# Optimization experiments

Measured on AMD Instinct MI355X. Metric: run time of the kernel, lower is better.

The kernel has to match this reference:

```python
import jax, jax.numpy as jnp
import numpy as np

EMBED_DIM = 768
N_HEADS = 12
TIME_RATIO = 0.5
HEAD_DIM = EMBED_DIM // N_HEADS          # 64
T_HEAD = int(HEAD_DIM * TIME_RATIO)      # 32 time dims per head
T_DIM = T_HEAD * N_HEADS                 # 384 time dims overall
EPS = 1e-5


def _ln(v, g, b):
    m = jnp.mean(v, axis=-1, keepdims=True)
    var = jnp.mean((v - m) ** 2, axis=-1, keepdims=True)
    return (v - m) * jax.lax.rsqrt(var + EPS) * g + b


def minkowski_ln(x, g_t, b_t, g_s, b_s):
    # normalize time-like and space-like channel groups separately
    xt, xs = x[..., :T_DIM], x[..., T_DIM:]
    return jnp.concatenate([_ln(xt, g_t, b_t), _ln(xs, g_s, b_s)], axis=-1)


def lorentz_attention(x, Wq, bq, Wk, bk, Wv, bv, Wo, bo):
    B, S, D = x.shape
    def heads(W, b):
        return (x @ W + b).reshape(B, S, N_HEADS, HEAD_DIM).transpose(0, 2, 1, 3)
    q, k, v = heads(Wq, bq), heads(Wk, bk), heads(Wv, bv)
    # Minkowski metric signature (-,...,-,+,...,+) within each head
    eta = jnp.concatenate([-jnp.ones((T_HEAD,), x.dtype), jnp.ones((HEAD_DIM - T_HEAD,), x.dtype)])
    logits = jnp.einsum('bhqd,bhkd->bhqk', q * eta, k) / np.sqrt(HEAD_DIM).astype(np.float32)
    attn = jax.nn.softmax(logits, axis=-1)
    o = jnp.einsum('bhqk,bhkd->bhqd', attn, v)
    o = o.transpose(0, 2, 1, 3).reshape(B, S, D)
    return o @ Wo + bo


def setup_inputs() -> dict:
    key = jax.random.key(0)
    ks = jax.random.split(key, 16)
    D, H4 = EMBED_DIM, EMBED_DIM * 4
    s = 0.02
    inp = {
        'x': jax.random.normal(ks[0], (2, 2048, D), jnp.float32),
        'Wq': jax.random.normal(ks[1], (D, D), jnp.float32) * s, 'bq': jnp.zeros((D,), jnp.float32),
        'Wk': jax.random.normal(ks[2], (D, D), jnp.float32) * s, 'bk': jnp.zeros((D,), jnp.float32),
        'Wv': jax.random.normal(ks[3], (D, D), jnp.float32) * s, 'bv': jnp.zeros((D,), jnp.float32),
        'Wo': jax.random.normal(ks[4], (D, D), jnp.float32) * s, 'bo': jnp.zeros((D,), jnp.float32),
        'g1t': jnp.ones((T_DIM,), jnp.float32), 'b1t': jnp.zeros((T_DIM,), jnp.float32),
        'g1s': jnp.ones((D - T_DIM,), jnp.float32), 'b1s': jnp.zeros((D - T_DIM,), jnp.float32),
        'W1': jax.random.normal(ks[5], (D, H4), jnp.float32) * s, 'bb1': jnp.zeros((H4,), jnp.float32),
        'W2': jax.random.normal(ks[6], (H4, D), jnp.float32) * s, 'bb2': jnp.zeros((D,), jnp.float32),
        'g2t': jnp.ones((T_DIM,), jnp.float32), 'b2t': jnp.zeros((T_DIM,), jnp.float32),
        'g2s': jnp.ones((D - T_DIM,), jnp.float32), 'b2s': jnp.zeros((D - T_DIM,), jnp.float32),
    }
    return inp


def reference(x, Wq, bq, Wk, bk, Wv, bv, Wo, bo,
              g1t, b1t, g1s, b1s, W1, bb1, W2, bb2,
              g2t, b2t, g2s, b2s):
    a = lorentz_attention(x, Wq, bq, Wk, bk, Wv, bv, Wo, bo)
    x = minkowski_ln(x + a, g1t, b1t, g1s, b1s)
    h = jax.nn.gelu(x @ W1 + bb1) @ W2 + bb2
    x = minkowski_ln(x + h, g2t, b2t, g2s, b2s)
    return x
```

## Files before the change

### kernel.cpp

```cpp
#include <hip/hip_runtime.h>
#include <cstddef>
#include <cstdint>

#define D_EMB  768
#define NHEAD  12
#define HDIM   64
#define THEAD  32
#define SEQ    2048
#define BATCH  2
#define NROW   (BATCH*SEQ)
#define HID4   3072

typedef unsigned short u16;
typedef __bf16 bf16x8 __attribute__((ext_vector_type(8)));
typedef float  f32x4  __attribute__((ext_vector_type(4)));
typedef unsigned short u16x8 __attribute__((ext_vector_type(8)));

__device__ __forceinline__ u16 f2bf(float f) {
    unsigned u = __builtin_bit_cast(unsigned, f);
    return (u16)((u + 0x7FFFu + ((u >> 16) & 1u)) >> 16);
}
__device__ __forceinline__ float bf2f(u16 h) {
    return __builtin_bit_cast(float, (unsigned)h << 16);
}

__device__ __forceinline__ void gload_lds16(const void* g, void* l) {
    __builtin_amdgcn_global_load_lds(
        reinterpret_cast<const __attribute__((address_space(1))) void*>(
            reinterpret_cast<uintptr_t>(g)),
        reinterpret_cast<__attribute__((address_space(3))) void*>(
            (uint32_t)reinterpret_cast<uintptr_t>(l)),
        16, 0, 0);
}

__device__ __forceinline__ void tcast(float (*t)[33], const float* __restrict__ W,
                                      u16* __restrict__ WT, int K, int M,
                                      int mt, int kt)
{
    const int m0 = mt * 32, k0 = kt * 32;
    const int tx = threadIdx.x & 31, ty = threadIdx.x >> 5;
#pragma unroll
    for (int i = 0; i < 32; i += 8)
        t[ty + i][tx] = W[(size_t)(k0 + ty + i) * M + m0 + tx];
    __syncthreads();
#pragma unroll
    for (int i = 0; i < 32; i += 8)
        WT[(size_t)(m0 + ty + i) * K + k0 + tx] = f2bf(t[tx][ty + i]);
}

__global__ __launch_bounds__(256)
void prep(const float* __restrict__ Wq, const float* __restrict__ Wk,
          const float* __restrict__ Wv, const float* __restrict__ Wo,
          const float* __restrict__ W1, const float* __restrict__ W2,
          const float* __restrict__ bq, const float* __restrict__ bk,
          const float* __restrict__ bv, const float* __restrict__ x,
          u16* __restrict__ WqkvoT, u16* __restrict__ W1T,
          u16* __restrict__ W2T, u16* __restrict__ xb,
          float* __restrict__ bqkv)
{
    __shared__ float t[32][33];
    const int bid = blockIdx.x;
    if (bid < 2304) {
        const int z = bid / 576, r = bid % 576;
        const float* W = z == 0 ? Wq : z == 1 ? Wk : z == 2 ? Wv : Wo;
        tcast(t, W, WqkvoT + (size_t)z * 768 * 768, 768, 768, r % 24, r / 24);
    } else if (bid < 4608) {
        const int r = bid - 2304;
        tcast(t, W1, W1T, 768, 3072, r % 96, r / 96);
    } else if (bid < 6912) {
        const int r = bid - 4608;
        tcast(t, W2, W2T, 3072, 768, r % 24, r / 24);
    } else if (bid < 8448) {
        const int i = (bid - 6912) * 2048 + threadIdx.x * 8;
        const float4 a = *reinterpret_cast<const float4*>(x + i);
        const float4 b = *reinterpret_cast<const float4*>(x + i + 4);
        u16x8 h;
        h[0] = f2bf(a.x); h[1] = f2bf(a.y); h[2] = f2bf(a.z); h[3] = f2bf(a.w);
        h[4] = f2bf(b.x); h[5] = f2bf(b.y); h[6] = f2bf(b.z); h[7] = f2bf(b.w);
        *reinterpret_cast<u16x8*>(xb + i) = h;
    } else {
        const int i = (bid - 8448) * 256 + threadIdx.x;
        if (i < 2304)
            bqkv[i] = i < 768 ? bq[i] : (i < 1536 ? bk[i - 768] : bv[i - 1536]);
    }
}

template<int EPI>
__global__ __launch_bounds__(256)
void gemm_bf16(const u16* __restrict__ A, const u16* __restrict__ B,
               const float* __restrict__ bias, void* __restrict__ Cp,
               u16* __restrict__ VTp, int K, int N)
{
    __shared__ u16 As[2][128 * 32];
    __shared__ u16 Bs[2][128 * 32];
    const int tid  = threadIdx.x;
    const int lane = tid & 63;
    const int w    = tid >> 6;
    const int m0 = blockIdx.x * 128, n0 = blockIdx.y * 128;
    const int wr = (w >> 1) << 6, wc = (w & 1) << 6;

    const int seg0 = (w << 11) + lane * 16;
    const int row0 = seg0 >> 6, cb0 = (seg0 & 63) >> 1;
    const int seg1 = seg0 + 1024;
    const int row1 = seg1 >> 6, cb1 = (seg1 & 63) >> 1;
    const u16* a0 = A + (size_t)(m0 + row0) * K + cb0;
    const u16* a1 = A + (size_t)(m0 + row1) * K + cb1;
    const u16* b0 = B + (size_t)(n0 + row0) * K + cb0;
    const u16* b1 = B + (size_t)(n0 + row1) * K + cb1;
    const int lo0 = (w * 2 + 0) << 9;
    const int lo1 = (w * 2 + 1) << 9;

    int aIdx[4], bIdx[4];
#pragma unroll
    for (int i = 0; i < 4; ++i) {
        aIdx[i] = (wr + i * 16 + (lane & 15)) * 32 + ((lane >> 4) << 3);
        bIdx[i] = (wc + i * 16 + (lane & 15)) * 32 + ((lane >> 4) << 3);
    }

    f32x4 acc[4][4];
#pragma unroll
    for (int i = 0; i < 4; ++i)
#pragma unroll
        for (int j = 0; j < 4; ++j)
#pragma unroll
            for (int q = 0; q < 4; ++q) acc[i][j][q] = 0.f;

    gload_lds16(a0, &As[0][lo0]);
    gload_lds16(a1, &As[0][lo1]);
    gload_lds16(b0, &Bs[0][lo0]);
    gload_lds16(b1, &Bs[0][lo1]);
    __syncthreads();

    int cur = 0;
    for (int k0 = 0; k0 < K; k0 += 32) {
        if (k0 + 32 < K) {
            gload_lds16(a0 + k0 + 32, &As[cur ^ 1][lo0]);
            gload_lds16(a1 + k0 + 32, &As[cur ^ 1][lo1]);
            gload_lds16(b0 + k0 + 32, &Bs[cur ^ 1][lo0]);
            gload_lds16(b1 + k0 + 32, &Bs[cur ^ 1][lo1]);
        }
        bf16x8 af[4], bv[4];
#pragma unroll
        for (int i = 0; i < 4; ++i)
            af[i] = *reinterpret_cast<const bf16x8*>(&As[cur][aIdx[i]]);
#pragma unroll
        for (int j = 0; j < 4; ++j)
            bv[j] = *reinterpret_cast<const bf16x8*>(&Bs[cur][bIdx[j]]);
#pragma unroll
        for (int i = 0; i < 4; ++i)
#pragma unroll
            for (int j = 0; j < 4; ++j)
                acc[i][j] = __builtin_amdgcn_mfma_f32_16x16x32_bf16(
                    af[i], bv[j], acc[i][j], 0, 0, 0);
        __syncthreads();
        cur ^= 1;
    }

#pragma unroll
    for (int i = 0; i < 4; ++i) {
#pragma unroll
        for (int q = 0; q < 4; ++q) {
            const int row = m0 + wr + i * 16 + ((lane >> 4) << 2) + q;
#pragma unroll
            for (int j = 0; j < 4; ++j) {
                const int col = n0 + wc + j * 16 + (lane & 15);
                float v = acc[i][j][q] + bias[col];
                if (EPI == 2) {
                    const float u3 = v * v * v;
                    v = 0.5f * v * (1.f + tanhf(0.7978845608028654f *
                                                (v + 0.044715f * u3)));
                    ((u16*)Cp)[(size_t)row * N + col] = f2bf(v);
                } else {
                    if (n0 < 1536) {
                        ((u16*)Cp)[(size_t)row * 1536 + col] = f2bf(v);
                    } else {
                        const int c2 = col - 1536;
                        const int hh = c2 >> 6, dd = c2 & 63;
                        const int bb = row >> 11, tok = row & 2047;
                        const int t = tok & 63;
                        const int p = ((t & 15) << 2) | (t >> 4);
                        VTp[((size_t)(bb * NHEAD + hh) * HDIM + dd) * SEQ
                            + (tok & ~63) + p] = f2bf(v);
                    }
                }
            }
        }
    }
}

__global__ __launch_bounds__(256)
void gemm_n64(const u16* __restrict__ A, const u16* __restrict__ B,
              const float* __restrict__ bias, float* __restrict__ C0,
              float* __restrict__ C1, int Khalf, int Ktot, int N)
{
    __shared__ u16 As[2][64 * 32];
    __shared__ u16 Bs[2][128 * 32];
    const int tid  = threadIdx.x;
    const int lane = tid & 63;
    const int w    = tid >> 6;
    const int l15  = lane & 15;
    const int g    = lane >> 4;
    const int m0 = blockIdx.x * 64, n0 = blockIdx.y * 128;
    const int zz = blockIdx.z;
    const int kbase = zz * Khalf;
    float* __restrict__ C = zz ? C1 : C0;

    const int segA = (w << 10) + lane * 16;
    const int rowA = segA >> 6, cbA = (segA & 63) >> 1;
    const u16* aP = A + (size_t)(m0 + rowA) * Ktot + kbase + cbA;
    const int loA = w << 9;
    const int seg0 = (w << 11) + lane * 16;
    const int row0 = seg0 >> 6, cb0 = (seg0 & 63) >> 1;
    const int seg1 = seg0 + 1024;
    const int row1 = seg1 >> 6, cb1 = (seg1 & 63) >> 1;
    const u16* b0 = B + (size_t)(n0 + row0) * Ktot + kbase + cb0;
    const u16* b1 = B + (size_t)(n0 + row1) * Ktot + kbase + cb1;
    const int lo0 = w << 10, lo1 = (w << 10) + 512;

    int aIdx[4], bIdx[2];
#pragma unroll
    for (int i = 0; i < 4; ++i) aIdx[i] = (i * 16 + l15) * 32 + (g << 3);
#pragma unroll
    for (int j = 0; j < 2; ++j) bIdx[j] = ((w << 5) + j * 16 + l15) * 32 + (g << 3);

    f32x4 acc[4][2];
#pragma unroll
    for (int i = 0; i < 4; ++i)
#pragma unroll
        for (int j = 0; j < 2; ++j)
#pragma unroll
            for (int q = 0; q < 4; ++q) acc[i][j][q] = 0.f;

    gload_lds16(aP, &As[0][loA]);
    gload_lds16(b0, &Bs[0][lo0]);
    gload_lds16(b1, &Bs[0][lo1]);
    __syncthreads();

    int cur = 0;
    for (int k0 = 0; k0 < Khalf; k0 += 32) {
        if (k0 + 32 < Khalf) {
            gload_lds16(aP + k0 + 32, &As[cur ^ 1][loA]);
            gload_lds16(b0 + k0 + 32, &Bs[cur ^ 1][lo0]);
            gload_lds16(b1 + k0 + 32, &Bs[cur ^ 1][lo1]);
        }
        bf16x8 af[4], bv[2];
#pragma unroll
        for (int i = 0; i < 4; ++i)
            af[i] = *reinterpret_cast<const bf16x8*>(&As[cur][aIdx[i]]);
#pragma unroll
        for (int j = 0; j < 2; ++j)
            bv[j] = *reinterpret_cast<const bf16x8*>(&Bs[cur][bIdx[j]]);
#pragma unroll
        for (int i = 0; i < 4; ++i)
#pragma unroll
            for (int j = 0; j < 2; ++j)
                acc[i][j] = __builtin_amdgcn_mfma_f32_16x16x32_bf16(
                    af[i], bv[j], acc[i][j], 0, 0, 0);
        __syncthreads();
        cur ^= 1;
    }

#pragma unroll
    for (int i = 0; i < 4; ++i) {
#pragma unroll
        for (int q = 0; q < 4; ++q) {
            const int row = m0 + i * 16 + (g << 2) + q;
#pragma unroll
            for (int j = 0; j < 2; ++j) {
                const int col = n0 + (w << 5) + j * 16 + l15;
                const float bb = zz ? 0.f : bias[col];
                C[(size_t)row * N + col] = acc[i][j][q] + bb;
            }
        }
    }
}

#define SM_SCALE 0.18033688011112042f

__global__ __launch_bounds__(256)
void attn_mfma(const u16* __restrict__ QK, const u16* __restrict__ VT,
               u16* __restrict__ O)
{
    __shared__ u16 Ks[2][64 * 64];
    __shared__ u16 Vs[2][64 * 64];
    __shared__ u16 Ps[64 * 72];

    const int tid  = threadIdx.x;
    const int lane = tid & 63;
    const int w    = tid >> 6;
    const int l15  = lane & 15;
    const int g    = lane >> 4;
    const int bh   = blockIdx.x;
    const int b    = bh / NHEAD, h = bh % NHEAD;
    const int q0   = blockIdx.y * 64;
    const int bS   = b * SEQ;

    bf16x8 aq[2];
    {
        const u16* Qg = QK + (size_t)(bS + q0 + (w << 4) + l15) * 1536 + h * HDIM;
#pragma unroll
        for (int kk = 0; kk < 2; ++kk) {
            const u16x8 hq = *reinterpret_cast<const u16x8*>(Qg + kk * 32 + g * 8);
            const float sc = (kk == 0) ? -SM_SCALE : SM_SCALE;
            u16x8 hs;
#pragma unroll
            for (int j = 0; j < 8; ++j)
                hs[j] = __builtin_bit_cast(u16, (__bf16)(bf2f(hq[j]) * sc));
            aq[kk] = __builtin_bit_cast(bf16x8, hs);
        }
    }

    const int rl = lane >> 3;
    const int cs = ((lane & 7) ^ rl) << 3;
    const u16* pK = QK + (size_t)(bS + 16 * w + rl) * 1536 + 768 + h * HDIM + cs;
    const u16* pV = VT + ((size_t)(b * NHEAD + h) * HDIM + 16 * w + rl) * SEQ + cs;

    int swz[2];
#pragma unroll
    for (int kk = 0; kk < 2; ++kk)
        swz[kk] = ((kk * 4 + g) ^ (l15 & 7)) << 3;

    bf16x8 vones;
    {
        u16x8 o16;
#pragma unroll
        for (int j = 0; j < 8; ++j) o16[j] = 0x3F80u;
        vones = __builtin_bit_cast(bf16x8, o16);
    }

    f32x4 accO[4];
#pragma unroll
    for (int n = 0; n < 4; ++n)
#pragma unroll
        for (int q = 0; q < 4; ++q) accO[n][q] = 0.f;
    f32x4 accS;
#pragma unroll
    for (int q = 0; q < 4; ++q) accS[q] = 0.f;

#define ATTN_STAGE(c, kt)                                                   \
    do {                                                                    \
        u16* dK = &Ks[c][w * 1024];                                         \
        u16* dV = &Vs[c][w * 1024];                                         \
        gload_lds16(pK + (size_t)(kt) * 1536,       dK);                    \
        gload_lds16(pK + (size_t)((kt) + 8) * 1536, dK + 512);              \
        gload_lds16(pV + (kt),           dV);                               \
        gload_lds16(pV + (kt) + 8 * SEQ, dV + 512);                         \
    } while (0)

    ATTN_STAGE(0, 0);
    __syncthreads();
    int cur = 0;

    for (int kt = 0; kt < SEQ; kt += 64) {
        if (kt + 64 < SEQ) ATTN_STAGE(cur ^ 1, kt + 64);

        f32x4 sac[4];
#pragma unroll
        for (int n = 0; n < 4; ++n) {
#pragma unroll
            for (int q = 0; q < 4; ++q) sac[n][q] = 0.f;
#pragma unroll
            for (int kk = 0; kk < 2; ++kk) {
                const bf16x8 bk = *reinterpret_cast<const bf16x8*>(
                    &Ks[cur][(n * 16 + l15) * 64 + swz[kk]]);
                sac[n] = __builtin_amdgcn_mfma_f32_16x16x32_bf16(
                    aq[kk], bk, sac[n], 0, 0, 0);
            }
        }

#pragma unroll
        for (int r4 = 0; r4 < 4; ++r4) {
            const int prow = (w << 4) + (g << 2) + r4;
            const float sv0 = __builtin_amdgcn_exp2f(sac[0][r4]);
            const float sv1 = __builtin_amdgcn_exp2f(sac[1][r4]);
            const float sv2 = __builtin_amdgcn_exp2f(sac[2][r4]);
            const float sv3 = __builtin_amdgcn_exp2f(sac[3][r4]);
            ushort4 pk4;
            pk4.x = __builtin_bit_cast(u16, (__bf16)sv0);
            pk4.y = __builtin_bit_cast(u16, (__bf16)sv1);
            pk4.z = __builtin_bit_cast(u16, (__bf16)sv2);
            pk4.w = __builtin_bit_cast(u16, (__bf16)sv3);
            *reinterpret_cast<ushort4*>(&Ps[prow * 72 + (l15 << 2)]) = pk4;
        }

        bf16x8 pa[2];
#pragma unroll
        for (int kk = 0; kk < 2; ++kk)
            pa[kk] = *reinterpret_cast<const bf16x8*>(
                &Ps[((w << 4) + l15) * 72 + kk * 32 + g * 8]);
#pragma unroll
        for (int n = 0; n < 4; ++n) {
#pragma unroll
            for (int kk = 0; kk < 2; ++kk) {
                const bf16x8 bv = *reinterpret_cast<const bf16x8*>(
                    &Vs[cur][(n * 16 + l15) * 64 + swz[kk]]);
                accO[n] = __builtin_amdgcn_mfma_f32_16x16x32_bf16(
                    pa[kk], bv, accO[n], 0, 0, 0);
            }
        }
#pragma unroll
        for (int kk = 0; kk < 2; ++kk)
            accS = __builtin_amdgcn_mfma_f32_16x16x32_bf16(
                pa[kk], vones, accS, 0, 0, 0);
        __syncthreads();
        cur ^= 1;
    }

#pragma unroll
    for (int r4 = 0; r4 < 4; ++r4) {
        const float inv = 1.f / accS[r4];
        const int qr = q0 + (w << 4) + (g << 2) + r4;
#pragma unroll
        for (int n = 0; n < 4; ++n)
            O[(size_t)(bS + qr) * D_EMB + h * HDIM + n * 16 + l15]
                = f2bf(accO[n][r4] * inv);
    }
#undef ATTN_STAGE
}

__global__ __launch_bounds__(256)
void mink_ln(const float* __restrict__ X, const float* __restrict__ R1,
             const float* __restrict__ R2,
             const float* __restrict__ gt, const float* __restrict__ bt,
             const float* __restrict__ gs, const float* __restrict__ bs,
             float* __restrict__ Out, u16* __restrict__ OutB, int nrows)
{
    const int wid  = (int)((blockIdx.x * 256 + threadIdx.x) >> 6);
    const int lane = threadIdx.x & 63;
    const int row  = wid >> 1, half = wid & 1;
    if (row >= nrows) return;

    const float* g  = half ? gs : gt;
    const float* bb = half ? bs : bt;
    const size_t base = (size_t)row * D_EMB + half * 384;

    float v[6];
    float sum = 0.f;
#pragma unroll
    for (int i = 0; i < 6; ++i) {
        const size_t e = base + i * 64 + lane;
        const float t = X[e] + R1[e] + R2[e];
        v[i] = t; sum += t;
    }
#pragma unroll
    for (int off = 32; off; off >>= 1) sum += __shfl_xor(sum, off);
    const float mean = sum * (1.f / 384.f);

    float ss = 0.f;
#pragma unroll
    for (int i = 0; i < 6; ++i) { const float d = v[i] - mean; ss += d * d; }
#pragma unroll
    for (int off = 32; off; off >>= 1) ss += __shfl_xor(ss, off);
    const float rstd = rsqrtf(ss * (1.f / 384.f) + 1e-5f);

#pragma unroll
    for (int i = 0; i < 6; ++i) {
        const int e = i * 64 + lane;
        const float o = (v[i] - mean) * rstd * g[e] + bb[e];
        Out[base + e] = o;
        if (OutB) OutB[base + e] = f2bf(o);
    }
}

extern "C" void kernel_launch(void* const* d_in, const int* in_sizes, int n_in,
                              void* d_out, int out_size, void* d_ws, size_t ws_size,
                              hipStream_t stream)
{
    const float* x   = (const float*)d_in[0];
    const float* Wq  = (const float*)d_in[1];
    const float* bq  = (const float*)d_in[2];
    const float* Wk  = (const float*)d_in[3];
    const float* bk  = (const float*)d_in[4];
    const float* Wv  = (const float*)d_in[5];
    const float* bv  = (const float*)d_in[6];
    const float* Wo  = (const float*)d_in[7];
    const float* bo  = (const float*)d_in[8];
    const float* g1t = (const float*)d_in[9];
    const float* b1t = (const float*)d_in[10];
    const float* g1s = (const float*)d_in[11];
    const float* b1s = (const float*)d_in[12];
    const float* W1  = (const float*)d_in[13];
    const float* bb1 = (const float*)d_in[14];
    const float* W2  = (const float*)d_in[15];
    const float* bb2 = (const float*)d_in[16];
    const float* g2t = (const float*)d_in[17];
    const float* b2t = (const float*)d_in[18];
    const float* g2s = (const float*)d_in[19];
    const float* b2s = (const float*)d_in[20];
    float* out = (float*)d_out;

    const size_t ND = (size_t)NROW * D_EMB;
    u16* WqkvoT = (u16*)d_ws;
    u16* W1T = WqkvoT + 2359296;
    u16* W2T = W1T + 2359296;
    u16* xb  = W2T + 2359296;
    u16* QKb = xb + ND;
    u16* VTb = QKb + (size_t)NROW * 1536;
    u16* Ab  = VTb + ND;
    u16* Hb  = QKb;
    float* QKf  = (float*)QKb;
    float* AoF  = (float*)(Ab + ND);
    float* bqkv = AoF;
    float* X1   = AoF + ND;

    const dim3 blk(256);

    prep<<<8457, blk, 0, stream>>>(Wq, Wk, Wv, Wo, W1, W2, bq, bk, bv, x,
                                   WqkvoT, W1T, W2T, xb, bqkv);

    gemm_bf16<3><<<dim3(32, 18), blk, 0, stream>>>(xb, WqkvoT, bqkv, QKb, VTb,
                                                   768, 2304);
    attn_mfma<<<dim3(BATCH * NHEAD, SEQ / 64), blk, 0, stream>>>(QKb, VTb, Ab);

    gemm_n64<<<dim3(64, 6, 2), blk, 0, stream>>>(
        Ab, WqkvoT + (size_t)2304 * 768, bo, AoF, QKf, 384, 768, 768);
    mink_ln<<<2048, blk, 0, stream>>>(x, AoF, QKf, g1t, b1t, g1s, b1s,
                                      X1, xb, NROW);
    gemm_bf16<2><<<dim3(32, 24), blk, 0, stream>>>(xb, W1T, bb1, Hb, nullptr,
                                                   768, 3072);
    gemm_n64<<<dim3(64, 6, 2), blk, 0, stream>>>(
        Hb, W2T, bb2, AoF, out, 1536, 3072, 768);
    mink_ln<<<2048, blk, 0, stream>>>(X1, AoF, out, g2t, b2t, g2s, b2s,
                                      out, nullptr, NROW);
}
```

Before: 191.0 us.

## Use fast GELU, hardware bf16 converts, MFMA priority hints, drop fp32 LN1 output

Replaces the tanh-based GELU with an equivalent sigmoid form built on exp2 and rcp intrinsics, swaps the manual rounding bf16 conversion for the native cast, and raises wave priority around the attention MFMA blocks. It also stops writing the fp32 copy of the first layernorm output and makes the second layernorm read the bf16 copy instead. That saves a full fp32 write and read of the activation. The cost is a small loss of precision in the residual path.

```diff
diff --git a/kernel.cpp b/kernel.cpp
--- a/kernel.cpp
+++ b/kernel.cpp
@@ -22,6 +22,9 @@
 }
 __device__ __forceinline__ float bf2f(u16 h) {
     return __builtin_bit_cast(float, (unsigned)h << 16);
+}
+__device__ __forceinline__ u16 cvt_bf(float f) {
+    return __builtin_bit_cast(u16, (__bf16)f);
 }
 
 __device__ __forceinline__ void gload_lds16(const void* g, void* l) {
@@ -166,13 +169,14 @@
                 const int col = n0 + wc + j * 16 + (lane & 15);
                 float v = acc[i][j][q] + bias[col];
                 if (EPI == 2) {
-                    const float u3 = v * v * v;
-                    v = 0.5f * v * (1.f + tanhf(0.7978845608028654f *
-                                                (v + 0.044715f * u3)));
-                    ((u16*)Cp)[(size_t)row * N + col] = f2bf(v);
+                    const float z = 1.5957691216057308f *
+                                    (v + 0.044715f * v * v * v);
+                    const float e = __builtin_amdgcn_exp2f(z * -1.4426950408889634f);
+                    v = v * __builtin_amdgcn_rcpf(1.f + e);
+                    ((u16*)Cp)[(size_t)row * N + col] = cvt_bf(v);
                 } else {
                     if (n0 < 1536) {
-                        ((u16*)Cp)[(size_t)row * 1536 + col] = f2bf(v);
+                        ((u16*)Cp)[(size_t)row * 1536 + col] = cvt_bf(v);
                     } else {
                         const int c2 = col - 1536;
                         const int hh = c2 >> 6, dd = c2 & 63;
@@ -180,7 +184,7 @@
                         const int t = tok & 63;
                         const int p = ((t & 15) << 2) | (t >> 4);
                         VTp[((size_t)(bb * NHEAD + hh) * HDIM + dd) * SEQ
-                            + (tok & ~63) + p] = f2bf(v);
+                            + (tok & ~63) + p] = cvt_bf(v);
                     }
                 }
             }
@@ -305,7 +309,7 @@
             u16x8 hs;
 #pragma unroll
             for (int j = 0; j < 8; ++j)
-                hs[j] = __builtin_bit_cast(u16, (__bf16)(bf2f(hq[j]) * sc));
+                hs[j] = cvt_bf(bf2f(hq[j]) * sc);
             aq[kk] = __builtin_bit_cast(bf16x8, hs);
         }
     }
@@ -355,6 +359,7 @@
         if (kt + 64 < SEQ) ATTN_STAGE(cur ^ 1, kt + 64);
 
         f32x4 sac[4];
+        __builtin_amdgcn_s_setprio(1);
 #pragma unroll
         for (int n = 0; n < 4; ++n) {
 #pragma unroll
@@ -367,6 +372,7 @@
                     aq[kk], bk, sac[n], 0, 0, 0);
             }
         }
+        __builtin_amdgcn_s_setprio(0);
 
 #pragma unroll
         for (int r4 = 0; r4 < 4; ++r4) {
@@ -376,10 +382,10 @@
             const float sv2 = __builtin_amdgcn_exp2f(sac[2][r4]);
             const float sv3 = __builtin_amdgcn_exp2f(sac[3][r4]);
             ushort4 pk4;
-            pk4.x = __builtin_bit_cast(u16, (__bf16)sv0);
-            pk4.y = __builtin_bit_cast(u16, (__bf16)sv1);
-            pk4.z = __builtin_bit_cast(u16, (__bf16)sv2);
-            pk4.w = __builtin_bit_cast(u16, (__bf16)sv3);
+            pk4.x = cvt_bf(sv0);
+            pk4.y = cvt_bf(sv1);
+            pk4.z = cvt_bf(sv2);
+            pk4.w = cvt_bf(sv3);
             *reinterpret_cast<ushort4*>(&Ps[prow * 72 + (l15 << 2)]) = pk4;
         }
 
@@ -388,6 +394,7 @@
         for (int kk = 0; kk < 2; ++kk)
             pa[kk] = *reinterpret_cast<const bf16x8*>(
                 &Ps[((w << 4) + l15) * 72 + kk * 32 + g * 8]);
+        __builtin_amdgcn_s_setprio(1);
 #pragma unroll
         for (int n = 0; n < 4; ++n) {
 #pragma unroll
@@ -402,6 +409,7 @@
         for (int kk = 0; kk < 2; ++kk)
             accS = __builtin_amdgcn_mfma_f32_16x16x32_bf16(
                 pa[kk], vones, accS, 0, 0, 0);
+        __builtin_amdgcn_s_setprio(0);
         __syncthreads();
         cur ^= 1;
     }
@@ -413,13 +421,14 @@
 #pragma unroll
         for (int n = 0; n < 4; ++n)
             O[(size_t)(bS + qr) * D_EMB + h * HDIM + n * 16 + l15]
-                = f2bf(accO[n][r4] * inv);
+                = cvt_bf(accO[n][r4] * inv);
     }
 #undef ATTN_STAGE
 }
 
+template<int XBF, int WF32>
 __global__ __launch_bounds__(256)
-void mink_ln(const float* __restrict__ X, const float* __restrict__ R1,
+void mink_ln(const void* __restrict__ Xp, const float* __restrict__ R1,
              const float* __restrict__ R2,
              const float* __restrict__ gt, const float* __restrict__ bt,
              const float* __restrict__ gs, const float* __restrict__ bs,
@@ -439,7 +448,8 @@
 #pragma unroll
     for (int i = 0; i < 6; ++i) {
         const size_t e = base + i * 64 + lane;
-        const float t = X[e] + R1[e] + R2[e];
+        const float xv = XBF ? bf2f(((const u16*)Xp)[e]) : ((const float*)Xp)[e];
+        const float t = xv + R1[e] + R2[e];
         v[i] = t; sum += t;
     }
 #pragma unroll
@@ -457,8 +467,8 @@
     for (int i = 0; i < 6; ++i) {
         const int e = i * 64 + lane;
         const float o = (v[i] - mean) * rstd * g[e] + bb[e];
-        Out[base + e] = o;
-        if (OutB) OutB[base + e] = f2bf(o);
+        if (WF32) Out[base + e] = o;
+        if (OutB) OutB[base + e] = cvt_bf(o);
     }
 }
 
@@ -501,7 +511,6 @@
     float* QKf  = (float*)QKb;
     float* AoF  = (float*)(Ab + ND);
     float* bqkv = AoF;
-    float* X1   = AoF + ND;
 
     const dim3 blk(256);
 
@@ -514,12 +523,12 @@
 
     gemm_n64<<<dim3(64, 6, 2), blk, 0, stream>>>(
         Ab, WqkvoT + (size_t)2304 * 768, bo, AoF, QKf, 384, 768, 768);
-    mink_ln<<<2048, blk, 0, stream>>>(x, AoF, QKf, g1t, b1t, g1s, b1s,
-                                      X1, xb, NROW);
+    mink_ln<0, 0><<<2048, blk, 0, stream>>>(x, AoF, QKf, g1t, b1t, g1s, b1s,
+                                            nullptr, xb, NROW);
     gemm_bf16<2><<<dim3(32, 24), blk, 0, stream>>>(xb, W1T, bb1, Hb, nullptr,
                                                    768, 3072);
     gemm_n64<<<dim3(64, 6, 2), blk, 0, stream>>>(
         Hb, W2T, bb2, AoF, out, 1536, 3072, 768);
-    mink_ln<<<2048, blk, 0, stream>>>(X1, AoF, out, g2t, b2t, g2s, b2s,
-                                      out, nullptr, NROW);
-}
+    mink_ln<1, 1><<<2048, blk, 0, stream>>>(xb, AoF, out, g2t, b2t, g2s, b2s,
+                                            out, nullptr, NROW);
+}
```

Result: faster. 179.8 us (-5.8%).
